# Kernel tuning notes

Measured on AMD Instinct MI355X. Metric: run time of the kernel, lower is better.

The kernel has to match this reference:

```python
import jax, jax.numpy as jnp
import numpy as np

B, C, H, W = 32, 64, 128, 128

def setup_inputs() -> dict:
    key = jax.random.key(0)
    k1, k2, k3, k4 = jax.random.split(key, 4)
    x = jax.random.normal(k1, (B, C, H, W), dtype=jnp.float32)
    theta = jax.random.normal(k2, (C, C), dtype=jnp.float32) * (6.0 / (C + C)) ** 0.5  # xavier-ish
    W_lin = jax.random.normal(k3, (C, C), dtype=jnp.float32) * (1.0 / C) ** 0.5
    b_lin = jax.random.normal(k4, (C,), dtype=jnp.float32) * 0.01
    return {"x": x, "theta": theta, "W_lin": W_lin, "b_lin": b_lin}

def reference(x, theta, W_lin, b_lin):
    b, c, h, w = x.shape
    # channel descriptor: global average pool -> [B, C]
    wvec = jnp.mean(x, axis=(2, 3))
    # pairwise diff and soft adjacency, batched over B
    diff = wvec[:, :, None] - wvec[:, None, :]              # [B, C, C]
    e = jnp.exp(-diff)
    T = jnp.abs(1.0 - e / (1.0 + e)) - 1.0                  # [B, C, C]
    A = 0.5 * (T + jnp.swapaxes(T, 1, 2)) * theta           # [B, C, C]
    # graph conv: A @ x_flat, relu
    x_flat = x.reshape(b, c, h * w)                         # [B, C, HW]
    Hmat = jax.nn.relu(jnp.einsum('bij,bjn->bin', A, x_flat))  # [B, C, HW]
    # Linear over channel dim applied to H.T: [B, HW, C]
    Hout = jnp.einsum('bin,ci->bnc', Hmat, W_lin) + b_lin   # [B, HW, C]
    # faithful to torch: H.view(C, h, w) is a raw row-major reshape of [HW, C]
    return Hout.reshape(b, c, h, w)
```

## Files before the change

### kernel.cpp

```cpp
#include <hip/hip_runtime.h>

static constexpr int Cc  = 64;
static constexpr int HWc = 16384;
static constexpr int Bc  = 32;
static constexpr int NT  = 256;


typedef _Float16 v8h __attribute__((ext_vector_type(8)));
typedef float    v4f __attribute__((ext_vector_type(4)));

union FragU { uint32_t u[4]; v8h h; };

__device__ inline uint32_t packf2(float lo, float hi) {
  union { _Float16 h[2]; uint32_t u; } r;
  r.h[0] = (_Float16)lo; r.h[1] = (_Float16)hi;
  return r.u;
}

__global__ void prep_weights(const float* __restrict__ theta,
                             const float* __restrict__ Wlin,
                             _Float16* __restrict__ M1h,
                             _Float16* __restrict__ Wh) {
  int t = blockIdx.x * 256 + threadIdx.x;
  if (t < Cc * Cc) {
    M1h[t] = (_Float16)(-0.5f * theta[t]);
    Wh[t]  = (_Float16)(Wlin[t]);
  }
}

__global__ __launch_bounds__(256) void fused_mfma(
    const float* __restrict__ x,
    const _Float16* __restrict__ M1h,
    const _Float16* __restrict__ Wh,
    const float* __restrict__ blin,
    float* __restrict__ out)
{
  __shared__ __align__(16) union {
    uint32_t xp[32][260];
    _Float16 p2[4][64][72];
  } lds;

  const int tid = threadIdx.x;
  const int b   = blockIdx.x >> 6;
  const int n0  = (blockIdx.x & 63) * NT;

  const float* xb = x + (size_t)b * Cc * HWc + n0;
#pragma unroll
  for (int rep = 0; rep < 8; ++rep) {
    const int chunk = rep * 256 + tid;
    const int p   = chunk >> 6;
    const int col = (chunk & 63) * 4;
    const float4 e = *(const float4*)(xb + (size_t)(2 * p)     * HWc + col);
    const float4 o = *(const float4*)(xb + (size_t)(2 * p + 1) * HWc + col);
    uint4 w;
    w.x = packf2(e.x, o.x); w.y = packf2(e.y, o.y);
    w.z = packf2(e.z, o.z); w.w = packf2(e.w, o.w);
    *(uint4*)&lds.xp[p][col] = w;
  }
  __syncthreads();

  const int wv   = tid >> 6;
  const int lq   = tid & 15;
  const int quad = (tid & 63) >> 4;
  const int nw   = wv * 64;

  FragU a1[4][2];
#pragma unroll
  for (int mt = 0; mt < 4; ++mt)
#pragma unroll
    for (int kt = 0; kt < 2; ++kt)
#pragma unroll
      for (int r = 0; r < 4; ++r)
        a1[mt][kt].u[r] = lds.xp[kt * 16 + quad * 4 + r][nw + mt * 16 + lq];

  const v8h* M1v = (const v8h*)M1h;
  v8h b1[4][2];
#pragma unroll
  for (int it = 0; it < 4; ++it)
#pragma unroll
    for (int kt = 0; kt < 2; ++kt)
      b1[it][kt] = M1v[(it * 16 + lq) * 8 + kt * 4 + quad];

  v4f acc1[4][4];
#pragma unroll
  for (int mt = 0; mt < 4; ++mt)
#pragma unroll
    for (int it = 0; it < 4; ++it) {
      v4f a = {0.f, 0.f, 0.f, 0.f};
#pragma unroll
      for (int kt = 0; kt < 2; ++kt)
        a = __builtin_amdgcn_mfma_f32_16x16x32_f16(a1[mt][kt].h, b1[it][kt], a, 0, 0, 0);
      acc1[mt][it] = a;
    }

  __syncthreads();

#pragma unroll
  for (int mt = 0; mt < 4; ++mt)
#pragma unroll
    for (int it = 0; it < 4; ++it)
#pragma unroll
      for (int r = 0; r < 4; ++r)
        lds.p2[wv][mt * 16 + quad * 4 + r][it * 16 + lq] =
            (_Float16)fmaxf(acc1[mt][it][r], 0.f);
  __syncthreads();

  const v8h* Whv = (const v8h*)Wh;
  v8h b2[4][2];
#pragma unroll
  for (int ct = 0; ct < 4; ++ct)
#pragma unroll
    for (int kt = 0; kt < 2; ++kt)
      b2[ct][kt] = Whv[(ct * 16 + lq) * 8 + kt * 4 + quad];

  float bias[4];
#pragma unroll
  for (int ct = 0; ct < 4; ++ct) bias[ct] = blin[ct * 16 + lq];

  const size_t outbase = ((size_t)b * HWc + n0 + nw) * Cc;
#pragma unroll
  for (int mt = 0; mt < 4; ++mt) {
    FragU a2[2];
#pragma unroll
    for (int kt = 0; kt < 2; ++kt)
      a2[kt].h = *(const v8h*)&lds.p2[wv][mt * 16 + lq][kt * 32 + quad * 8];
#pragma unroll
    for (int ct = 0; ct < 4; ++ct) {
      v4f a = {bias[ct], bias[ct], bias[ct], bias[ct]};
#pragma unroll
      for (int kt = 0; kt < 2; ++kt)
        a = __builtin_amdgcn_mfma_f32_16x16x32_f16(a2[kt].h, b2[ct][kt], a, 0, 0, 0);
#pragma unroll
      for (int r = 0; r < 4; ++r)
        out[outbase + (size_t)(mt * 16 + quad * 4 + r) * Cc + ct * 16 + lq] = a[r];
    }
  }
}

extern "C" void kernel_launch(void* const* d_in, const int* in_sizes, int n_in,
                              void* d_out, int out_size, void* d_ws, size_t ws_size,
                              hipStream_t stream) {
  const float* x     = (const float*)d_in[0];
  const float* theta = (const float*)d_in[1];
  const float* W_lin = (const float*)d_in[2];
  const float* b_lin = (const float*)d_in[3];
  float* out = (float*)d_out;

  _Float16* M1h = (_Float16*)d_ws;
  _Float16* Wh  = M1h + Cc * Cc;

  prep_weights<<<(Cc * Cc + 255) / 256, 256, 0, stream>>>(theta, W_lin, M1h, Wh);

  const int nblocks = Bc * HWc / NT;
  fused_mfma<<<nblocks, 256, 0, stream>>>(x, M1h, Wh, b_lin, out);
}
```

Before: 239.8 us.

## Swap MFMA operand roles to load x directly and store output vectorized

The x-to-LDS staging pass is removed. Each wave now loads x columns straight from global memory into B fragments, with the weights acting as the A operand, and packs pairs of values to fp16 using cvt_pkrtz. The transposed layout lets each lane write four contiguous output floats as one v4f store instead of scalar stores, and it removes one of the block barriers. The risk is that the direct global loads are scalar 4-byte reads spread across channel rows, which could coalesce worse than the earlier float4 staging.

```diff
diff --git a/kernel.cpp b/kernel.cpp
--- a/kernel.cpp
+++ b/kernel.cpp
@@ -3,18 +3,17 @@
 static constexpr int Cc  = 64;
 static constexpr int HWc = 16384;
 static constexpr int Bc  = 32;
-static constexpr int NT  = 256;
 
 
 typedef _Float16 v8h __attribute__((ext_vector_type(8)));
+typedef __fp16   pk2 __attribute__((ext_vector_type(2)));
 typedef float    v4f __attribute__((ext_vector_type(4)));
 
 union FragU { uint32_t u[4]; v8h h; };
+union H2U   { pk2 h; uint32_t u; };
 
-__device__ inline uint32_t packf2(float lo, float hi) {
-  union { _Float16 h[2]; uint32_t u; } r;
-  r.h[0] = (_Float16)lo; r.h[1] = (_Float16)hi;
-  return r.u;
+__device__ inline uint32_t pkf2(float a, float b) {
+  H2U t; t.h = __builtin_amdgcn_cvt_pkrtz(a, b); return t.u;
 }
 
 __global__ void prep_weights(const float* __restrict__ theta,
@@ -28,111 +27,91 @@
   }
 }
 
-__global__ __launch_bounds__(256) void fused_mfma(
+__global__ __launch_bounds__(256) void fused_mfma2(
     const float* __restrict__ x,
     const _Float16* __restrict__ M1h,
     const _Float16* __restrict__ Wh,
     const float* __restrict__ blin,
     float* __restrict__ out)
 {
-  __shared__ __align__(16) union {
-    uint32_t xp[32][260];
-    _Float16 p2[4][64][72];
-  } lds;
+  __shared__ __align__(16) _Float16 p2[4][64][72];
 
   const int tid = threadIdx.x;
+  const int wv  = tid >> 6;
+  const int lq  = tid & 15;
+  const int q   = (tid & 63) >> 4;
+
   const int b   = blockIdx.x >> 6;
-  const int n0  = (blockIdx.x & 63) * NT;
-
-  const float* xb = x + (size_t)b * Cc * HWc + n0;
-#pragma unroll
-  for (int rep = 0; rep < 8; ++rep) {
-    const int chunk = rep * 256 + tid;
-    const int p   = chunk >> 6;
-    const int col = (chunk & 63) * 4;
-    const float4 e = *(const float4*)(xb + (size_t)(2 * p)     * HWc + col);
-    const float4 o = *(const float4*)(xb + (size_t)(2 * p + 1) * HWc + col);
-    uint4 w;
-    w.x = packf2(e.x, o.x); w.y = packf2(e.y, o.y);
-    w.z = packf2(e.z, o.z); w.w = packf2(e.w, o.w);
-    *(uint4*)&lds.xp[p][col] = w;
-  }
-  __syncthreads();
-
-  const int wv   = tid >> 6;
-  const int lq   = tid & 15;
-  const int quad = (tid & 63) >> 4;
-  const int nw   = wv * 64;
-
-  FragU a1[4][2];
-#pragma unroll
-  for (int mt = 0; mt < 4; ++mt)
-#pragma unroll
-    for (int kt = 0; kt < 2; ++kt)
-#pragma unroll
-      for (int r = 0; r < 4; ++r)
-        a1[mt][kt].u[r] = lds.xp[kt * 16 + quad * 4 + r][nw + mt * 16 + lq];
+  const int n0  = (blockIdx.x & 63) * 256 + wv * 64;
+  const float* xb = x + (size_t)b * Cc * HWc;
 
   const v8h* M1v = (const v8h*)M1h;
-  v8h b1[4][2];
+  v8h a1[4][2];
 #pragma unroll
   for (int it = 0; it < 4; ++it)
 #pragma unroll
     for (int kt = 0; kt < 2; ++kt)
-      b1[it][kt] = M1v[(it * 16 + lq) * 8 + kt * 4 + quad];
+      a1[it][kt] = M1v[(it * 16 + lq) * 8 + kt * 4 + q];
 
-  v4f acc1[4][4];
 #pragma unroll
-  for (int mt = 0; mt < 4; ++mt)
+  for (int nt = 0; nt < 4; ++nt) {
+    const int n = n0 + nt * 16 + lq;
+    FragU b1[2];
+#pragma unroll
+    for (int kt = 0; kt < 2; ++kt)
+#pragma unroll
+      for (int r = 0; r < 4; ++r) {
+        const int c0 = kt * 32 + q * 8 + 2 * r;
+        b1[kt].u[r] = pkf2(xb[(size_t)c0 * HWc + n],
+                           xb[(size_t)(c0 + 1) * HWc + n]);
+      }
+    v4f acc[4];
 #pragma unroll
     for (int it = 0; it < 4; ++it) {
       v4f a = {0.f, 0.f, 0.f, 0.f};
 #pragma unroll
       for (int kt = 0; kt < 2; ++kt)
-        a = __builtin_amdgcn_mfma_f32_16x16x32_f16(a1[mt][kt].h, b1[it][kt], a, 0, 0, 0);
-      acc1[mt][it] = a;
+        a = __builtin_amdgcn_mfma_f32_16x16x32_f16(a1[it][kt], b1[kt].h, a, 0, 0, 0);
+      acc[it] = a;
     }
+#pragma unroll
+    for (int it = 0; it < 4; ++it) {
+      uint2 w;
+      w.x = pkf2(fmaxf(acc[it][0], 0.f), fmaxf(acc[it][1], 0.f));
+      w.y = pkf2(fmaxf(acc[it][2], 0.f), fmaxf(acc[it][3], 0.f));
+      *(uint2*)&p2[wv][nt * 16 + lq][it * 16 + 4 * q] = w;
+    }
+  }
+
+  const v8h* Whv = (const v8h*)Wh;
+  v8h a2[4][2];
+#pragma unroll
+  for (int ct = 0; ct < 4; ++ct)
+#pragma unroll
+    for (int kt = 0; kt < 2; ++kt)
+      a2[ct][kt] = Whv[(ct * 16 + lq) * 8 + kt * 4 + q];
+
+  float4 bias4[4];
+#pragma unroll
+  for (int ct = 0; ct < 4; ++ct)
+    bias4[ct] = *(const float4*)(blin + ct * 16 + q * 4);
 
   __syncthreads();
 
 #pragma unroll
-  for (int mt = 0; mt < 4; ++mt)
-#pragma unroll
-    for (int it = 0; it < 4; ++it)
-#pragma unroll
-      for (int r = 0; r < 4; ++r)
-        lds.p2[wv][mt * 16 + quad * 4 + r][it * 16 + lq] =
-            (_Float16)fmaxf(acc1[mt][it][r], 0.f);
-  __syncthreads();
-
-  const v8h* Whv = (const v8h*)Wh;
-  v8h b2[4][2];
-#pragma unroll
-  for (int ct = 0; ct < 4; ++ct)
+  for (int nt = 0; nt < 4; ++nt) {
+    const int n = n0 + nt * 16 + lq;
+    v8h b2[2];
 #pragma unroll
     for (int kt = 0; kt < 2; ++kt)
-      b2[ct][kt] = Whv[(ct * 16 + lq) * 8 + kt * 4 + quad];
-
-  float bias[4];
-#pragma unroll
-  for (int ct = 0; ct < 4; ++ct) bias[ct] = blin[ct * 16 + lq];
-
-  const size_t outbase = ((size_t)b * HWc + n0 + nw) * Cc;
-#pragma unroll
-  for (int mt = 0; mt < 4; ++mt) {
-    FragU a2[2];
-#pragma unroll
-    for (int kt = 0; kt < 2; ++kt)
-      a2[kt].h = *(const v8h*)&lds.p2[wv][mt * 16 + lq][kt * 32 + quad * 8];
+      b2[kt] = *(const v8h*)&p2[wv][nt * 16 + lq][kt * 32 + q * 8];
 #pragma unroll
     for (int ct = 0; ct < 4; ++ct) {
-      v4f a = {bias[ct], bias[ct], bias[ct], bias[ct]};
+      v4f a = {bias4[ct].x, bias4[ct].y, bias4[ct].z, bias4[ct].w};
 #pragma unroll
       for (int kt = 0; kt < 2; ++kt)
-        a = __builtin_amdgcn_mfma_f32_16x16x32_f16(a2[kt].h, b2[ct][kt], a, 0, 0, 0);
-#pragma unroll
-      for (int r = 0; r < 4; ++r)
-        out[outbase + (size_t)(mt * 16 + quad * 4 + r) * Cc + ct * 16 + lq] = a[r];
+        a = __builtin_amdgcn_mfma_f32_16x16x32_f16(a2[ct][kt], b2[kt], a, 0, 0, 0);
+      *(v4f*)(out + ((size_t)b * HWc + n) * Cc + ct * 16 + q * 4) = a;
     }
   }
 }
@@ -151,6 +130,6 @@
 
   prep_weights<<<(Cc * Cc + 255) / 256, 256, 0, stream>>>(theta, W_lin, M1h, Wh);
 
-  const int nblocks = Bc * HWc / NT;
-  fused_mfma<<<nblocks, 256, 0, stream>>>(x, M1h, Wh, b_lin, out);
+  const int nblocks = Bc * HWc / 256;
+  fused_mfma2<<<nblocks, 256, 0, stream>>>(x, M1h, Wh, b_lin, out);
 }
```

New measurement: 260.7 us. 1.09x slower.
